# Optimization experiments

Hardware: AMD Instinct MI355X
Metric: run time of the kernel (lower is better)

Reference implementation:

```python
import jax, jax.numpy as jnp
import numpy as np

B, S, D = 4, 2048, 1024
H = 16
HD = D // H  # head_dim = 64


def setup_inputs() -> dict:
    key = jax.random.key(0)
    ks = jax.random.split(key, 5)
    scale = 1.0 / np.sqrt(D)
    return {
        "x": jax.random.normal(ks[0], (B, S, D), dtype=jnp.float32),
        "Wq": jax.random.normal(ks[1], (D, D), dtype=jnp.float32) * scale,
        "Wk": jax.random.normal(ks[2], (D, D), dtype=jnp.float32) * scale,
        "Wv": jax.random.normal(ks[3], (D, D), dtype=jnp.float32) * scale,
        "Wo": jax.random.normal(ks[4], (D, D), dtype=jnp.float32) * scale,
        "bo": jnp.zeros((D,), dtype=jnp.float32),
    }


def reference(x, Wq, Wk, Wv, Wo, bo):
    b, s, d = x.shape
    # project and split heads: [b, h, s, hd]
    q = (x @ Wq).reshape(b, s, H, HD).transpose(0, 2, 1, 3)
    k = (x @ Wk).reshape(b, s, H, HD).transpose(0, 2, 1, 3)
    v = (x @ Wv).reshape(b, s, H, HD).transpose(0, 2, 1, 3)
    # scores: [b, h, s, s]
    scores = jnp.einsum("bhqd,bhkd->bhqk", q, k)
    # NOTE: original uses tril(diagonal=1) -> allows one future token (off-by-one)
    mask = jnp.tril(jnp.ones((s, s), dtype=bool), k=1)
    scores = jnp.where(mask, scores, -jnp.inf)
    attn = jax.nn.softmax(scores / np.sqrt(HD), axis=-1)
    # dropout p=0.0 (deterministic baseline): identity
    ctx = jnp.einsum("bhqk,bhkd->bhqd", attn, v)
    ctx = ctx.transpose(0, 2, 1, 3).reshape(b, s, d)
    return ctx @ Wo + bo
```

## Files before the change

kernel.cpp:

```cpp
#include <hip/hip_runtime.h>
#include <hip/hip_bf16.h>

#define Bq 4
#define Sq 2048
#define Dq 1024
#define Hq 16
#define HDq 64
#define Mq (Bq*Sq)

typedef unsigned short u16;
typedef __attribute__((ext_vector_type(8))) __bf16 b16x8;
typedef __attribute__((ext_vector_type(4))) float f32x4;
typedef __attribute__((ext_vector_type(4))) unsigned int u32x4;

__device__ inline float bf2f(u16 h){ union{unsigned u; float f;} v; v.u = ((unsigned)h)<<16; return v.f; }
__device__ inline u16 f2bf(float f){ union{float f; unsigned u;} v; v.f=f; unsigned r = v.u + 0x7FFFu + ((v.u>>16)&1u); return (u16)(r>>16); }
__device__ inline u16 truncbf(float f){ union{float f; unsigned u;} v; v.f=f; return (u16)(v.u>>16); }
__device__ inline float ld_elem(const void* p, size_t i, int isf32){
  return isf32 ? ((const float*)p)[i] : bf2f(((const u16*)p)[i]);
}
__device__ inline void ld16(const u16* g, u16* l){
  __builtin_amdgcn_global_load_lds((const __attribute__((address_space(1))) void*)g,
                                   (__attribute__((address_space(3))) void*)l, 16, 0, 0);
}

#if __has_builtin(__builtin_amdgcn_exp2f)
#define EXP2(x) __builtin_amdgcn_exp2f(x)
#else
#define EXP2(x) __expf((x)*0.69314718056f)
#endif
#define SCALE_LOG2E 0.18033688011112042f

__global__ void detect_dtype(const unsigned* __restrict__ x, int* __restrict__ flag){
  __shared__ int cnt;
  if(threadIdx.x==0) cnt=0;
  __syncthreads();
  int local=0;
  for(int i=threadIdx.x;i<2048;i+=256){
    unsigned w = x[i];
    if(((w>>7)&0xFFu)>=0x90u) local++;
    if(((w>>23)&0xFFu)>=0x90u) local++;
  }
  atomicAdd(&cnt, local);
  __syncthreads();
  if(threadIdx.x==0) *flag = (cnt>64) ? 1 : 0;
}

__global__ __launch_bounds__(256) void convert_x(const void* __restrict__ x, u16* __restrict__ xc,
                                                 const int* __restrict__ flag, int n){
  const int f = *flag;
  int i = (blockIdx.x*256 + threadIdx.x)*8;
  if(i>=n) return;
  if(f){
    const float* xf=(const float*)x;
    #pragma unroll
    for(int j=0;j<8;j++) xc[i+j] = f2bf(xf[i+j]);
  } else {
    *(u32x4*)&xc[i] = *(const u32x4*)((const u16*)x + i);
  }
}

__global__ __launch_bounds__(256) void transpose_w(
    const void* __restrict__ W0, const void* __restrict__ W1,
    const void* __restrict__ W2, const void* __restrict__ W3,
    u16* __restrict__ T0, u16* __restrict__ T1,
    u16* __restrict__ T2, u16* __restrict__ T3,
    const int* __restrict__ flag){
  __shared__ u16 tile[64][65];
  const int f = *flag;
  const int z = blockIdx.z;
  const void* src = (z==0)?W0:(z==1)?W1:(z==2)?W2:W3;
  u16*       dst = (z==0)?T0:(z==1)?T1:(z==2)?T2:T3;
  const int t = threadIdx.x;
  const int k0 = blockIdx.x*64, n0 = blockIdx.y*64;
  #pragma unroll
  for(int r=0;r<16;r++){
    int row = r*4 + (t>>6), col = t&63;
    tile[row][col] = f2bf(ld_elem(src, (size_t)(k0+row)*Dq + n0 + col, f));
  }
  __syncthreads();
  #pragma unroll
  for(int r=0;r<16;r++){
    int row = r*4 + (t>>6), col = t&63;
    dst[(size_t)(n0+row)*Dq + k0 + col] = tile[col][row];
  }
}

template<int MODE>
__global__ __launch_bounds__(512, 2) void gemm256(
    const u16* __restrict__ A, const u16* __restrict__ Bt,
    u16* __restrict__ O0, u16* __restrict__ O1, u16* __restrict__ O2,
    void* __restrict__ Og, const void* __restrict__ bias, const int* __restrict__ flag){
  __shared__ u16 Al[3][256*64];
  __shared__ u16 Bl[3][128*64];
  const int f = (MODE==1) ? *flag : 0;
  const int t = threadIdx.x;
  const int lane = t & 63, wave = t >> 6;
  const int quad = lane >> 4, l16 = lane & 15;
  const int wr = wave >> 1, wc = wave & 1;
  int L  = blockIdx.x + blockIdx.y*gridDim.x;
  int k8 = L & 7, ii = L >> 3;
  int mPerX = gridDim.y >> 3;
  const int NB = 8;
  int cells = NB * mPerX;
  int nb  = ii / cells, rem = ii - nb*cells;
  int mg  = rem >> 3, nn = rem & 7;
  const int m0 = (k8*mPerX + mg)*256, n0 = (nb*NB + nn)*128;
  const int NT = Dq/64;

  f32x4 acc[4][4] = {};

  auto stage = [&](int kt, int s){
    const int k0 = kt<<6;
    #pragma unroll
    for(int r=0;r<4;r++){
      int idx = t + (r<<9);
      int row = idx>>3, g = idx&7;
      int csw = (g ^ (row&7))<<3;
      ld16(&A[(size_t)(m0+row)*Dq + k0 + csw], &Al[s][idx*8]);
    }
    #pragma unroll
    for(int r=0;r<2;r++){
      int idx = t + (r<<9);
      int row = idx>>3, g = idx&7;
      int csw = (g ^ (row&7))<<3;
      ld16(&Bt[(size_t)(n0+row)*Dq + k0 + csw], &Bl[s][idx*8]);
    }
  };

  auto compute = [&](int s){
    const u16* As = &Al[s][0];
    const u16* Bs = &Bl[s][0];
    #pragma unroll
    for(int ks=0;ks<2;ks++){
      b16x8 af[4], bfr[4];
      #pragma unroll
      for(int i=0;i<4;i++){
        int row = wr*64 + i*16 + l16;
        af[i] = *(const b16x8*)&As[row*64 + ((((ks<<2)+quad) ^ (row&7))<<3)];
      }
      #pragma unroll
      for(int j=0;j<4;j++){
        int row = wc*64 + j*16 + l16;
        bfr[j] = *(const b16x8*)&Bs[row*64 + ((((ks<<2)+quad) ^ (row&7))<<3)];
      }
      __builtin_amdgcn_s_setprio(1);
      #pragma unroll
      for(int i=0;i<4;i++)
        #pragma unroll
        for(int j=0;j<4;j++)
          acc[i][j] = __builtin_amdgcn_mfma_f32_16x16x32_bf16(af[i], bfr[j], acc[i][j], 0,0,0);
      __builtin_amdgcn_s_setprio(0);
    }
  };

  stage(0,0);
  stage(1,1);
  asm volatile("s_waitcnt vmcnt(6)" ::: "memory");
  __builtin_amdgcn_s_barrier();
  __builtin_amdgcn_sched_barrier(0);

  int s0=0, s1=1, s2=2;
  for(int tt=0; tt<NT-2; ++tt){
    stage(tt+2, s2);
    compute(s0);
    asm volatile("s_waitcnt vmcnt(6)" ::: "memory");
    __builtin_amdgcn_s_barrier();
    __builtin_amdgcn_sched_barrier(0);
    int x=s0; s0=s1; s1=s2; s2=x;
  }
  compute(s0);
  asm volatile("s_waitcnt vmcnt(0)" ::: "memory");
  __builtin_amdgcn_s_barrier();
  __builtin_amdgcn_sched_barrier(0);
  compute(s1);

  #pragma unroll
  for(int i=0;i<4;i++){
    #pragma unroll
    for(int j=0;j<4;j++){
      int n = n0 + wc*64 + j*16 + l16;
      #pragma unroll
      for(int r=0;r<4;r++){
        int m = m0 + wr*64 + i*16 + quad*4 + r;
        float c = acc[i][j][r];
        if (MODE==1){
          float c2 = c + ld_elem(bias, n, f);
          if (f) ((float*)Og)[(size_t)m*Dq + n] = c2;
          else   ((u16*)Og)[(size_t)m*Dq + n]   = f2bf(c2);
        } else {
          int z = n >> 10, nn2 = n & 1023;
          int b = m >> 11, s = m & 2047;
          int h = nn2 >> 6, hd = nn2 & 63;
          if (z==0)      O0[(((size_t)(b*Hq + h))*Sq + s)*HDq + hd] = f2bf(c*SCALE_LOG2E);
          else if (z==1) O1[(((size_t)(b*Hq + h))*Sq + s)*HDq + hd] = f2bf(c);
          else           O2[(((size_t)(b*Hq + h))*HDq + hd)*Sq + s] = f2bf(c);
        }
      }
    }
  }
}

__global__ __launch_bounds__(256) void flash_attn(
    const u16* __restrict__ Q, const u16* __restrict__ K,
    const u16* __restrict__ VT, u16* __restrict__ C){
  __shared__ u16 Kt[128*64];
  __shared__ u16 Vt[64*128];
  __shared__ u16 Pl[4][16][72];
  const int t = threadIdx.x;
  const int lane = t&63, wave = t>>6, quad = lane>>4, l16 = lane&15;
  int L  = blockIdx.x + blockIdx.y*gridDim.x;
  int k8 = L & 7, ii = L >> 3;
  const int bh = k8*8 + (ii>>4);
  const int p  = ii & 15;
  const int b = bh >> 4, h = bh & 15;
  const int qt[2] = { p, 31 - p };
  int nk[2];
  #pragma unroll
  for(int tt=0;tt<2;tt++){ int v = qt[tt]+2; nk[tt] = (v<32)?v:32; }
  const int nrounds = (nk[1]+1)>>1;
  const u16* Qh = Q  + (size_t)bh*Sq*HDq;
  const u16* Kh = K  + (size_t)bh*Sq*HDq;
  const u16* Vh = VT + (size_t)bh*HDq*Sq;

  b16x8 aq[2][2];
  #pragma unroll
  for(int tt=0;tt<2;tt++){
    const u16* qp = Qh + (size_t)(qt[tt]*64 + wave*16 + l16)*HDq + quad*8;
    aq[tt][0] = *(const b16x8*)qp;
    aq[tt][1] = *(const b16x8*)(qp + 32);
  }
  b16x8 vone;
  #pragma unroll
  for(int i=0;i<8;i++) vone[i] = (__bf16)1.0f;

  const f32x4 fzero = {0.f,0.f,0.f,0.f};
  f32x4 Oa[2][4]; f32x4 lacc[2];
  #pragma unroll
  for(int tt=0;tt<2;tt++){ lacc[tt]=fzero; for(int j=0;j<4;j++) Oa[tt][j]=fzero; }

  for(int kt2=0; kt2<nrounds; kt2++){
    __syncthreads();
    #pragma unroll
    for(int r=0;r<4;r++){
      int idx = t + (r<<8);
      int row = idx>>3, g = idx&7;
      int csw = (g ^ (row&7))<<3;
      ld16(Kh + (size_t)(kt2*128+row)*HDq + csw, Kt + idx*8);
    }
    #pragma unroll
    for(int r=0;r<4;r++){
      int idx = t + (r<<8);
      int row = idx>>4, g = idx&15;
      int csw = (g ^ (row&15))<<3;
      ld16(Vh + (size_t)row*Sq + (size_t)kt2*128 + csw, Vt + idx*8);
    }
    __syncthreads();

    #pragma unroll
    for(int half=0; half<2; half++){
      const int kt = kt2*2 + half;
      #pragma unroll
      for(int tt=0;tt<2;tt++){
        if (kt >= nk[tt]) continue;
        const int qq0 = qt[tt]*64;
        f32x4 sc[4];
        #pragma unroll
        for(int jn=0;jn<4;jn++){
          int krow = half*64 + jn*16 + l16;
          const u16* kp = &Kt[krow*64];
          f32x4 s = fzero;
          b16x8 bk0 = *(const b16x8*)&kp[((quad     ^ (krow&7))<<3)];
          b16x8 bk1 = *(const b16x8*)&kp[(((quad+4) ^ (krow&7))<<3)];
          s = __builtin_amdgcn_mfma_f32_16x16x32_bf16(aq[tt][0], bk0, s, 0,0,0);
          s = __builtin_amdgcn_mfma_f32_16x16x32_bf16(aq[tt][1], bk1, s, 0,0,0);
          sc[jn] = s;
        }
        if (kt < qt[tt]) {
          #pragma unroll
          for(int jn=0;jn<4;jn++)
            #pragma unroll
            for(int r=0;r<4;r++)
              Pl[wave][quad*4+r][jn*16+l16] = truncbf(EXP2(sc[jn][r]));
        } else {
          const int qbase = qq0 + wave*16 + quad*4;
          #pragma unroll
          for(int jn=0;jn<4;jn++){
            int kg = kt*64 + jn*16 + l16;
            #pragma unroll
            for(int r=0;r<4;r++){
              float sv = sc[jn][r];
              if (kg > qbase + r + 1) sv = -__builtin_inff();
              Pl[wave][quad*4+r][jn*16+l16] = truncbf(EXP2(sv));
            }
          }
        }
        #pragma unroll
        for(int ks=0;ks<2;ks++){
          b16x8 ap = *(const b16x8*)&Pl[wave][l16][ks*32 + quad*8];
          int glog = half*8 + ks*4 + quad;
          #pragma unroll
          for(int jd=0;jd<4;jd++){
            int hd = jd*16 + l16;
            b16x8 bv = *(const b16x8*)&Vt[hd*128 + ((glog ^ (hd&15))<<3)];
            Oa[tt][jd] = __builtin_amdgcn_mfma_f32_16x16x32_bf16(ap, bv, Oa[tt][jd], 0,0,0);
          }
          lacc[tt] = __builtin_amdgcn_mfma_f32_16x16x32_bf16(ap, vone, lacc[tt], 0,0,0);
        }
      }
    }
  }
  #pragma unroll
  for(int tt=0;tt<2;tt++){
    const int qq0 = qt[tt]*64;
    #pragma unroll
    for(int r=0;r<4;r++){
      int s = qq0 + wave*16 + quad*4 + r;
      float inv = 1.0f / lacc[tt][r];
      #pragma unroll
      for(int jd=0;jd<4;jd++)
        C[((size_t)(b*Sq + s))*Dq + h*HDq + jd*16 + l16] = f2bf(Oa[tt][jd][r]*inv);
    }
  }
}

extern "C" void kernel_launch(void* const* d_in, const int* in_sizes, int n_in,
                              void* d_out, int out_size, void* d_ws, size_t ws_size,
                              hipStream_t stream){
  const void* x  = d_in[0];
  const void* Wq = d_in[1];
  const void* Wk = d_in[2];
  const void* Wv = d_in[3];
  const void* Wo = d_in[4];
  const void* bo = d_in[5];

  char* ws = (char*)d_ws;
  size_t off = 0;
  auto wsalloc = [&](size_t bytes)->void*{
    void* p = ws + off; off += (bytes + 255) & ~(size_t)255; return p;
  };
  int* flag = (int*)wsalloc(256);
  u16* WqT = (u16*)wsalloc((size_t)Dq*Dq*2);
  u16* WkT = (u16*)wsalloc((size_t)Dq*Dq*2);
  u16* WvT = (u16*)wsalloc((size_t)Dq*Dq*2);
  u16* WoT = (u16*)wsalloc((size_t)Dq*Dq*2);
  u16* xc  = (u16*)wsalloc((size_t)Mq*Dq*2);
  u16* Qb  = (u16*)wsalloc((size_t)Mq*Dq*2);
  u16* Kb  = (u16*)wsalloc((size_t)Mq*Dq*2);
  u16* VTb = (u16*)wsalloc((size_t)Mq*Dq*2);
  u16* Cb  = (u16*)wsalloc((size_t)Mq*Dq*2);

  detect_dtype<<<1, 256, 0, stream>>>((const unsigned*)x, flag);
  convert_x<<<dim3(Mq*Dq/8/256), 256, 0, stream>>>(x, xc, flag, Mq*Dq);
  transpose_w<<<dim3(16,16,4), 256, 0, stream>>>(Wq,Wk,Wv,Wo, WqT,WkT,WvT,WoT, flag);
  gemm256<0><<<dim3(24, Mq/256), 512, 0, stream>>>(xc, WqT, Qb,Kb,VTb, nullptr, nullptr, flag);
  flash_attn<<<dim3(16, Bq*Hq), 256, 0, stream>>>(Qb, Kb, VTb, Cb);
  gemm256<1><<<dim3(Dq/128, Mq/256), 512, 0, stream>>>(Cb, WoT, nullptr,nullptr,nullptr, d_out, bo, flag);
}
```

Measured before the change: 210.9 us.

## Rewrite GEMM as 128x256 tile with half-K ping-pong staging interleaved with MFMAs

Swaps the GEMM block tile from 256x128 to 128x256, with waves arranged 2x4 instead of 4x2. The three-stage 64-wide K buffer becomes double-buffered 32-wide K halves. Global-to-LDS loads for the next half-tiles are issued between MFMA groups, so memory traffic overlaps with matrix math at a finer grain. The aim is to hide load latency with less LDS, at the cost of more barriers per K step and a different block-to-tile mapping in both GEMM launches.

```diff
diff --git a/kernel.cpp b/kernel.cpp
--- a/kernel.cpp
+++ b/kernel.cpp
@@ -87,93 +87,115 @@
 }
 
 template<int MODE>
-__global__ __launch_bounds__(512, 2) void gemm256(
+__global__ __launch_bounds__(512, 2) void gemm8p(
     const u16* __restrict__ A, const u16* __restrict__ Bt,
     u16* __restrict__ O0, u16* __restrict__ O1, u16* __restrict__ O2,
     void* __restrict__ Og, const void* __restrict__ bias, const int* __restrict__ flag){
-  __shared__ u16 Al[3][256*64];
-  __shared__ u16 Bl[3][128*64];
+  __shared__ u16 Asl[2][2][128*32];
+  __shared__ u16 Bsl[2][2][256*32];
   const int f = (MODE==1) ? *flag : 0;
   const int t = threadIdx.x;
   const int lane = t & 63, wave = t >> 6;
   const int quad = lane >> 4, l16 = lane & 15;
-  const int wr = wave >> 1, wc = wave & 1;
+  const int wr = wave >> 2, wc = wave & 3;
   int L  = blockIdx.x + blockIdx.y*gridDim.x;
   int k8 = L & 7, ii = L >> 3;
-  int mPerX = gridDim.y >> 3;
-  const int NB = 8;
-  int cells = NB * mPerX;
-  int nb  = ii / cells, rem = ii - nb*cells;
-  int mg  = rem >> 3, nn = rem & 7;
-  const int m0 = (k8*mPerX + mg)*256, n0 = (nb*NB + nn)*128;
+  int nb = ii >> 5, rem = ii & 31;
+  int mg = rem >> 2, nn = rem & 3;
+  const int m0 = (k8*8 + mg)*128, n0 = (nb*4 + nn)*256;
   const int NT = Dq/64;
 
   f32x4 acc[4][4] = {};
 
-  auto stage = [&](int kt, int s){
-    const int k0 = kt<<6;
-    #pragma unroll
-    for(int r=0;r<4;r++){
-      int idx = t + (r<<9);
-      int row = idx>>3, g = idx&7;
-      int csw = (g ^ (row&7))<<3;
-      ld16(&A[(size_t)(m0+row)*Dq + k0 + csw], &Al[s][idx*8]);
-    }
+  auto stageA = [&](int T, int kh){
+    int row = t>>2, gp = t&3, gl = gp ^ ((row>>1)&3);
+    ld16(&A[(size_t)(m0+row)*Dq + (T<<6) + kh*32 + gl*8], &Asl[T&1][kh][t*8]);
+  };
+  auto stageB = [&](int T, int kh){
     #pragma unroll
     for(int r=0;r<2;r++){
       int idx = t + (r<<9);
-      int row = idx>>3, g = idx&7;
-      int csw = (g ^ (row&7))<<3;
-      ld16(&Bt[(size_t)(n0+row)*Dq + k0 + csw], &Bl[s][idx*8]);
-    }
-  };
-
-  auto compute = [&](int s){
-    const u16* As = &Al[s][0];
-    const u16* Bs = &Bl[s][0];
-    #pragma unroll
-    for(int ks=0;ks<2;ks++){
-      b16x8 af[4], bfr[4];
-      #pragma unroll
-      for(int i=0;i<4;i++){
-        int row = wr*64 + i*16 + l16;
-        af[i] = *(const b16x8*)&As[row*64 + ((((ks<<2)+quad) ^ (row&7))<<3)];
-      }
-      #pragma unroll
-      for(int j=0;j<4;j++){
-        int row = wc*64 + j*16 + l16;
-        bfr[j] = *(const b16x8*)&Bs[row*64 + ((((ks<<2)+quad) ^ (row&7))<<3)];
-      }
-      __builtin_amdgcn_s_setprio(1);
-      #pragma unroll
-      for(int i=0;i<4;i++)
-        #pragma unroll
-        for(int j=0;j<4;j++)
-          acc[i][j] = __builtin_amdgcn_mfma_f32_16x16x32_bf16(af[i], bfr[j], acc[i][j], 0,0,0);
-      __builtin_amdgcn_s_setprio(0);
-    }
-  };
-
-  stage(0,0);
-  stage(1,1);
-  asm volatile("s_waitcnt vmcnt(6)" ::: "memory");
-  __builtin_amdgcn_s_barrier();
-  __builtin_amdgcn_sched_barrier(0);
-
-  int s0=0, s1=1, s2=2;
-  for(int tt=0; tt<NT-2; ++tt){
-    stage(tt+2, s2);
-    compute(s0);
-    asm volatile("s_waitcnt vmcnt(6)" ::: "memory");
+      int row = idx>>2, gp = idx&3, gl = gp ^ ((row>>1)&3);
+      ld16(&Bt[(size_t)(n0+row)*Dq + (T<<6) + kh*32 + gl*8], &Bsl[T&1][kh][idx*8]);
+    }
+  };
+  auto ldA = [&](int pb, int kh, int i)->b16x8{
+    int row = wr*64 + i*16 + l16;
+    return *(const b16x8*)&Asl[pb][kh][row*32 + ((quad ^ ((row>>1)&3))<<3)];
+  };
+  auto ldB = [&](int pb, int kh, int j)->b16x8{
+    int row = wc*64 + j*16 + l16;
+    return *(const b16x8*)&Bsl[pb][kh][row*32 + ((quad ^ ((row>>1)&3))<<3)];
+  };
+  #define MFMA_BF16 __builtin_amdgcn_mfma_f32_16x16x32_bf16
+
+  stageA(0,0); stageB(0,0); stageA(0,1); stageB(0,1); stageA(1,0); stageB(1,0);
+
+  for(int T=0; T<NT-1; ++T){
+    const int pb = T&1;
+    asm volatile("s_waitcnt vmcnt(3)" ::: "memory");
     __builtin_amdgcn_s_barrier();
     __builtin_amdgcn_sched_barrier(0);
-    int x=s0; s0=s1; s1=s2; s2=x;
-  }
-  compute(s0);
-  asm volatile("s_waitcnt vmcnt(0)" ::: "memory");
-  __builtin_amdgcn_s_barrier();
-  __builtin_amdgcn_sched_barrier(0);
-  compute(s1);
+    stageA(T+1, 1);
+    {
+      b16x8 a0=ldA(pb,0,0), a1=ldA(pb,0,1), a2=ldA(pb,0,2), a3=ldA(pb,0,3);
+      b16x8 b0=ldB(pb,0,0), b1=ldB(pb,0,1);
+      __builtin_amdgcn_s_setprio(1);
+      acc[0][0]=MFMA_BF16(a0,b0,acc[0][0],0,0,0); acc[1][0]=MFMA_BF16(a1,b0,acc[1][0],0,0,0);
+      acc[2][0]=MFMA_BF16(a2,b0,acc[2][0],0,0,0); acc[3][0]=MFMA_BF16(a3,b0,acc[3][0],0,0,0);
+      acc[0][1]=MFMA_BF16(a0,b1,acc[0][1],0,0,0); acc[1][1]=MFMA_BF16(a1,b1,acc[1][1],0,0,0);
+      acc[2][1]=MFMA_BF16(a2,b1,acc[2][1],0,0,0); acc[3][1]=MFMA_BF16(a3,b1,acc[3][1],0,0,0);
+      __builtin_amdgcn_s_setprio(0);
+      b16x8 b2=ldB(pb,0,2), b3=ldB(pb,0,3);
+      stageB(T+1, 1);
+      __builtin_amdgcn_s_setprio(1);
+      acc[0][2]=MFMA_BF16(a0,b2,acc[0][2],0,0,0); acc[1][2]=MFMA_BF16(a1,b2,acc[1][2],0,0,0);
+      acc[2][2]=MFMA_BF16(a2,b2,acc[2][2],0,0,0); acc[3][2]=MFMA_BF16(a3,b2,acc[3][2],0,0,0);
+      acc[0][3]=MFMA_BF16(a0,b3,acc[0][3],0,0,0); acc[1][3]=MFMA_BF16(a1,b3,acc[1][3],0,0,0);
+      acc[2][3]=MFMA_BF16(a2,b3,acc[2][3],0,0,0); acc[3][3]=MFMA_BF16(a3,b3,acc[3][3],0,0,0);
+      __builtin_amdgcn_s_setprio(0);
+    }
+    __builtin_amdgcn_s_barrier();
+    __builtin_amdgcn_sched_barrier(0);
+    if(T < NT-2) stageA(T+2, 0);
+    {
+      b16x8 a0=ldA(pb,1,0), a1=ldA(pb,1,1), a2=ldA(pb,1,2), a3=ldA(pb,1,3);
+      b16x8 b0=ldB(pb,1,0), b1=ldB(pb,1,1);
+      __builtin_amdgcn_s_setprio(1);
+      acc[0][0]=MFMA_BF16(a0,b0,acc[0][0],0,0,0); acc[1][0]=MFMA_BF16(a1,b0,acc[1][0],0,0,0);
+      acc[2][0]=MFMA_BF16(a2,b0,acc[2][0],0,0,0); acc[3][0]=MFMA_BF16(a3,b0,acc[3][0],0,0,0);
+      acc[0][1]=MFMA_BF16(a0,b1,acc[0][1],0,0,0); acc[1][1]=MFMA_BF16(a1,b1,acc[1][1],0,0,0);
+      acc[2][1]=MFMA_BF16(a2,b1,acc[2][1],0,0,0); acc[3][1]=MFMA_BF16(a3,b1,acc[3][1],0,0,0);
+      __builtin_amdgcn_s_setprio(0);
+      b16x8 b2=ldB(pb,1,2), b3=ldB(pb,1,3);
+      if(T < NT-2) stageB(T+2, 0);
+      __builtin_amdgcn_s_setprio(1);
+      acc[0][2]=MFMA_BF16(a0,b2,acc[0][2],0,0,0); acc[1][2]=MFMA_BF16(a1,b2,acc[1][2],0,0,0);
+      acc[2][2]=MFMA_BF16(a2,b2,acc[2][2],0,0,0); acc[3][2]=MFMA_BF16(a3,b2,acc[3][2],0,0,0);
+      acc[0][3]=MFMA_BF16(a0,b3,acc[0][3],0,0,0); acc[1][3]=MFMA_BF16(a1,b3,acc[1][3],0,0,0);
+      acc[2][3]=MFMA_BF16(a2,b3,acc[2][3],0,0,0); acc[3][3]=MFMA_BF16(a3,b3,acc[3][3],0,0,0);
+      __builtin_amdgcn_s_setprio(0);
+    }
+  }
+  {
+    const int pb = (NT-1)&1;
+    asm volatile("s_waitcnt vmcnt(0)" ::: "memory");
+    __builtin_amdgcn_s_barrier();
+    __builtin_amdgcn_sched_barrier(0);
+    #pragma unroll
+    for(int kh=0; kh<2; ++kh){
+      b16x8 a0=ldA(pb,kh,0), a1=ldA(pb,kh,1), a2=ldA(pb,kh,2), a3=ldA(pb,kh,3);
+      b16x8 b0=ldB(pb,kh,0), b1=ldB(pb,kh,1), b2=ldB(pb,kh,2), b3=ldB(pb,kh,3);
+      acc[0][0]=MFMA_BF16(a0,b0,acc[0][0],0,0,0); acc[1][0]=MFMA_BF16(a1,b0,acc[1][0],0,0,0);
+      acc[2][0]=MFMA_BF16(a2,b0,acc[2][0],0,0,0); acc[3][0]=MFMA_BF16(a3,b0,acc[3][0],0,0,0);
+      acc[0][1]=MFMA_BF16(a0,b1,acc[0][1],0,0,0); acc[1][1]=MFMA_BF16(a1,b1,acc[1][1],0,0,0);
+      acc[2][1]=MFMA_BF16(a2,b1,acc[2][1],0,0,0); acc[3][1]=MFMA_BF16(a3,b1,acc[3][1],0,0,0);
+      acc[0][2]=MFMA_BF16(a0,b2,acc[0][2],0,0,0); acc[1][2]=MFMA_BF16(a1,b2,acc[1][2],0,0,0);
+      acc[2][2]=MFMA_BF16(a2,b2,acc[2][2],0,0,0); acc[3][2]=MFMA_BF16(a3,b2,acc[3][2],0,0,0);
+      acc[0][3]=MFMA_BF16(a0,b3,acc[0][3],0,0,0); acc[1][3]=MFMA_BF16(a1,b3,acc[1][3],0,0,0);
+      acc[2][3]=MFMA_BF16(a2,b3,acc[2][3],0,0,0); acc[3][3]=MFMA_BF16(a3,b3,acc[3][3],0,0,0);
+    }
+  }
 
   #pragma unroll
   for(int i=0;i<4;i++){
@@ -199,6 +221,7 @@
       }
     }
   }
+  #undef MFMA_BF16
 }
 
 __global__ __launch_bounds__(256) void flash_attn(
@@ -353,7 +376,7 @@
   detect_dtype<<<1, 256, 0, stream>>>((const unsigned*)x, flag);
   convert_x<<<dim3(Mq*Dq/8/256), 256, 0, stream>>>(x, xc, flag, Mq*Dq);
   transpose_w<<<dim3(16,16,4), 256, 0, stream>>>(Wq,Wk,Wv,Wo, WqT,WkT,WvT,WoT, flag);
-  gemm256<0><<<dim3(24, Mq/256), 512, 0, stream>>>(xc, WqT, Qb,Kb,VTb, nullptr, nullptr, flag);
+  gemm8p<0><<<dim3(12, Mq/128), 512, 0, stream>>>(xc, WqT, Qb,Kb,VTb, nullptr, nullptr, flag);
   flash_attn<<<dim3(16, Bq*Hq), 256, 0, stream>>>(Qb, Kb, VTb, Cb);
-  gemm256<1><<<dim3(Dq/128, Mq/256), 512, 0, stream>>>(Cb, WoT, nullptr,nullptr,nullptr, d_out, bo, flag);
-}
+  gemm8p<1><<<dim3(4, Mq/128), 512, 0, stream>>>(Cb, WoT, nullptr,nullptr,nullptr, d_out, bo, flag);
+}
```

Measured after the change: 218.7 us. 3.7% more time.
